# Kernel tuning notes

Measured on AMD Instinct MI355X. Metric: run time of the kernel, lower is better.

Reference implementation:

```python
import jax, jax.numpy as jnp
import numpy as np

# Dimensions
F = 512      # features = len(in_degrees)
D = 64
S, B, N = 1, 64, 256   # outer sample dim, hyper-batch, points per batch element
C = 128      # conditioner (phi) feature dim
P = F * F + F  # flat params per batch element: weight + bias


def _mask():
    # hidden-layer MADE degrees: arange(F) % max(1, D-1) + min(1, D-1)
    d = jnp.arange(F) % (D - 1) + 1
    # MaskedLinear hidden mask: out_degrees[:, None] >= in_degrees[None, :]
    # (the torch code reshapes the square [F,F] mask, which is an identity
    #  memory reshape, so element (i, j) = (d[i] >= d[j]))
    return (d[:, None] >= d[None, :]).astype(jnp.float32)


def setup_inputs() -> dict:
    key = jax.random.key(0)
    k1, k2, k3, k4 = jax.random.split(key, 4)
    return {
        "inputs": jax.random.normal(k1, (S, B, N, F), jnp.float32),
        "phi": jax.random.normal(k2, (S, B, C), jnp.float32),
        "Wc": jax.random.normal(k3, (P, C), jnp.float32) * 0.02,
        "bc": jax.random.normal(k4, (P,), jnp.float32) * 0.02,
    }


def reference(inputs, phi, Wc, bc):
    # Conditioner net: linear hypernetwork phi -> flat per-batch params.
    params = jnp.einsum('sbc,pc->sbp', phi, Wc) + bc          # [S,B,P]
    w = params[..., : F * F].reshape(S, B, F, F)               # [S,B,F_in,F_out]
    b = params[..., F * F : F * F + F]                         # [S,B,F]
    mw = w * _mask()                                           # masked per-batch weights

    # Residual block (no batch norm, dropout p=0): act -> masked linear (x2) -> residual
    t = jax.nn.relu(inputs)
    t = jnp.einsum('sbni,sbik->sbnk', t, mw) + b[:, :, None, :]
    t = jax.nn.relu(t)
    # Both MaskedLinear layers split the SAME conditioner output, so they share
    # (w, b); only the masks could differ, and with these degrees they coincide.
    t = jnp.einsum('sbni,sbik->sbnk', t, mw) + b[:, :, None, :]
    return inputs + t
```

## Files before the change

### kernel.cpp

```cpp
#include <hip/hip_runtime.h>
#include <hip/hip_bf16.h>

#define F_   512
#define FF_  (512 * 512)
#define C_   128

typedef __attribute__((ext_vector_type(4))) float f32x4;
typedef __attribute__((ext_vector_type(8))) short s16x8;
typedef __attribute__((ext_vector_type(4))) unsigned short u16x4;

__device__ __forceinline__ unsigned short f2bf(float f) {
    union { __hip_bfloat16 h; unsigned short u; } c;
    c.h = __float2bfloat16(f);
    return c.u;
}

__device__ __forceinline__ s16x8 pack8(f32x4 lo, f32x4 hi) {
    s16x8 r;
    r[0] = (short)f2bf(lo[0]); r[1] = (short)f2bf(lo[1]);
    r[2] = (short)f2bf(lo[2]); r[3] = (short)f2bf(lo[3]);
    r[4] = (short)f2bf(hi[0]); r[5] = (short)f2bf(hi[1]);
    r[6] = (short)f2bf(hi[2]); r[7] = (short)f2bf(hi[3]);
    return r;
}

#define GLDS16(gp, lp)                                                         \
    __builtin_amdgcn_global_load_lds(                                          \
        (const __attribute__((address_space(1))) void*)(gp),                   \
        (__attribute__((address_space(3))) void*)(lp), 16, 0, 0)

__global__ __launch_bounds__(256) void k0_prepack(
    const float* __restrict__ phi, unsigned short* __restrict__ phiP)
{
    const int t = threadIdx.x;
#pragma unroll
    for (int j = 0; j < 4; ++j) {
        int e = (j << 8) + t;
        int lane = e & 63, mk = e >> 6;
        int m = mk >> 2, kk = mk & 3;
        int brow = lane & 15, quad = lane >> 4;
        const float* p = phi + ((m << 4) + brow) * C_ + kk * 32 + (quad << 3);
        s16x8 v = pack8(*(const f32x4*)p, *(const f32x4*)(p + 4));
        *(s16x8*)&phiP[e << 3] = v;
    }
}

__global__ __launch_bounds__(256, 2) void k1_params(
    const unsigned short* __restrict__ phiP, const float* __restrict__ Wc,
    const float* __restrict__ bc, unsigned short* __restrict__ wT,
    float* __restrict__ biasWS, const float* __restrict__ phi)
{
    const int blk = blockIdx.x;
    const int tid = threadIdx.x;

    if (blk >= 512) {
        int g = ((blk - 512) << 8) + tid;
        int k = g >> 6, b = g & 63;
        const f32x4* w4 = (const f32x4*)(Wc + (size_t)(FF_ + k) * C_);
        const f32x4* p4 = (const f32x4*)(phi + b * C_);
        float acc = bc[FF_ + k];
#pragma unroll
        for (int c = 0; c < 32; ++c) {
            f32x4 a = w4[c], q = p4[c];
            acc += a[0]*q[0] + a[1]*q[1] + a[2]*q[2] + a[3]*q[3];
        }
        biasWS[(b << 9) + k] = acc;
        return;
    }

    __shared__ __align__(16) char stg[2][32768];
    __shared__ __align__(16) unsigned short trans[4][1280];
    __shared__ float bcs[64 * 9];

    const int lane = tid & 63, wave = tid >> 6, quad = lane >> 4;
    const int i0 = (blk >> 6) << 6;
    const int k0 = (blk & 63) << 3;

    {
        int il = tid >> 2, kp = (tid & 3) << 1;
        const float* s = bc + (size_t)(i0 + il) * F_ + k0 + kp;
        bcs[il * 9 + kp]     = s[0];
        bcs[il * 9 + kp + 1] = s[1];
    }

    s16x8 bfr[4];
#pragma unroll
    for (int kk = 0; kk < 4; ++kk)
        bfr[kk] = *(const s16x8*)&phiP[((((wave << 2) + kk) << 6) | lane) << 3];

    int dcell[4][4];
#pragma unroll
    for (int mt = 0; mt < 4; ++mt)
#pragma unroll
        for (int rr = 0; rr < 4; ++rr)
            dcell[mt][rr] = (i0 + mt * 16 + (quad << 2) + rr) % 63;
    int dmax[4];
#pragma unroll
    for (int mt = 0; mt < 4; ++mt) {
        int a = (i0 + mt * 16) % 63;
        dmax[mt] = (a + 15 >= 63) ? 62 : a + 15;
    }

    int irow[8], drow[8], swj[8];
#pragma unroll
    for (int j = 0; j < 8; ++j) {
        int rl = (wave << 4) + (j << 1) + (lane >> 5);
        irow[j] = i0 + rl;
        drow[j] = (i0 + rl) % 63;
        swj[j]  = ((lane & 31) << 4) ^ ((rl & 7) << 4);
    }
    const int idup = i0 + ((62 - (i0 % 63)) + 63) % 63;

    auto STAGE = [&](int t, int buf) {
        const int k = k0 + t, dk = (k0 + t) % 63;
#pragma unroll
        for (int j = 0; j < 8; ++j) {
            int isel = (drow[j] >= dk) ? irow[j] : idup;
            const char* src = (const char*)Wc
                            + ((size_t)(isel * F_ + k) << 9) + swj[j];
            GLDS16(src, stg[buf] + (((wave << 4) + (j << 1)) << 9));
        }
    };

    STAGE(0, 0);
    __syncthreads();

    const int swz = (lane & 7) << 4;

#pragma unroll
    for (int t = 0; t < 8; ++t) {
        if (t < 7) STAGE(t + 1, (t + 1) & 1);

        const int dk = (k0 + t) % 63;
        const char* sb = stg[t & 1];
        unsigned short* trw = trans[wave];

#pragma unroll
        for (int mt = 0; mt < 4; ++mt) {
            const int tpos = ((lane & 15) * 160
                           + ((mt * 32 + (quad << 3)) ^ swz)) >> 1;
            if (dmax[mt] >= dk) {
                f32x4 acc = (f32x4){0.f, 0.f, 0.f, 0.f};
                const char* rowb = sb + ((mt * 16 + (lane & 15)) << 9);
#pragma unroll
                for (int kk = 0; kk < 4; ++kk) {
                    int x = ((kk << 7) + (quad << 5)) ^ swz;
                    f32x4 lo = *(const f32x4*)(rowb + x);
                    f32x4 hi = *(const f32x4*)(rowb + (x ^ 16));
                    acc = __builtin_amdgcn_mfma_f32_16x16x32_bf16(
                        pack8(lo, hi), bfr[kk], acc, 0, 0, 0);
                }
                u16x4 v;
#pragma unroll
                for (int rr = 0; rr < 4; ++rr) {
                    float bv = bcs[(mt * 16 + (quad << 2) + rr) * 9 + t];
                    v[rr] = (dcell[mt][rr] >= dk)
                          ? f2bf(acc[rr] + bv) : (unsigned short)0;
                }
                *(u16x4*)&trw[tpos] = v;
            } else {
                *(u16x4*)&trw[tpos] = (u16x4){0, 0, 0, 0};
            }
        }

#pragma unroll
        for (int h = 0; h < 2; ++h) {
            int bl = (h << 3) + (lane >> 3), r = lane & 7;
            int rr2 = r ^ (bl & 7);
            s16x8 v = *(const s16x8*)&trw[bl * 80 + (rr2 << 3)];
            unsigned short* dst = wT
                + (((size_t)(((wave << 4) + bl) << 9) + k0 + t) << 9)
                + i0 + (r << 3);
            *(s16x8*)dst = v;
        }

        if (t < 7) {
            asm volatile("s_waitcnt vmcnt(2)" ::: "memory");
            __builtin_amdgcn_s_barrier();
        }
    }
}

#define SMEM_BOFF 66560
#define CHUNK_B   32768
#define SMEM_TOT  (66560 + 2 * 32768)

__global__ __launch_bounds__(512) void k2_apply(
    const float* __restrict__ X, const unsigned short* __restrict__ wT,
    const float* __restrict__ biasWS, float* __restrict__ out)
{
    extern __shared__ char smem[];
    unsigned short* A_lds = (unsigned short*)smem;

    const int blk = blockIdx.x;
    const int sw  = ((blk & 7) << 5) + (blk >> 3);
    const int b   = sw >> 2;
    const int n0  = (sw & 3) << 6;

    const int tid = threadIdx.x, lane = tid & 63, wave = tid >> 6;
    const int wn = wave >> 2, wk = wave & 3;

    const float* Xb = X + (((size_t)(b * 256 + n0)) << 9);
    float*       Ob = out + (((size_t)(b * 256 + n0)) << 9);
    const unsigned short* wTb = wT + ((size_t)b << 18);

    float biasr[8];
#pragma unroll
    for (int nt = 0; nt < 8; ++nt)
        biasr[nt] = biasWS[(b << 9) + (wk << 7) + (nt << 4) + (lane & 15)];

    {
        const f32x4* X4 = (const f32x4*)Xb;
#pragma unroll
        for (int j = 0; j < 16; ++j) {
            int f = (j << 9) + tid;
            int row = f >> 7, c4 = f & 127;
            f32x4 v = X4[f];
            u16x4 h;
#pragma unroll
            for (int e = 0; e < 4; ++e) h[e] = f2bf(fmaxf(v[e], 0.f));
            *(u16x4*)&A_lds[row * 520 + (c4 << 2)] = h;
        }
    }

    const int srcslot = ((lane & 3) ^ ((lane >> 3) & 3)) << 3;

    f32x4 acc[2][8];

    for (int phase = 0; phase < 2; ++phase) {
#pragma unroll
        for (int mt = 0; mt < 2; ++mt)
#pragma unroll
            for (int nt = 0; nt < 8; ++nt) acc[mt][nt] = (f32x4){0.f, 0.f, 0.f, 0.f};

#pragma unroll
        for (int g = 0; g < 4; ++g) {
            int krow = (wave << 6) + (g << 4) + (lane >> 2);
            const unsigned short* src = wTb + ((size_t)krow << 9) + srcslot;
            char* lp = smem + SMEM_BOFF + (((wave << 6) + (g << 4)) << 6);
            GLDS16(src, lp);
        }
        asm volatile("s_waitcnt vmcnt(0)" ::: "memory");
        __syncthreads();

        for (int c = 0; c < 16; ++c) {
            const int cur = c & 1;
            if (c < 15) {
                const int i0n = (c + 1) << 5;
#pragma unroll
                for (int g = 0; g < 4; ++g) {
                    int krow = (wave << 6) + (g << 4) + (lane >> 2);
                    const unsigned short* src = wTb + ((size_t)krow << 9) + i0n + srcslot;
                    char* lp = smem + SMEM_BOFF + (cur ^ 1) * CHUNK_B
                             + (((wave << 6) + (g << 4)) << 6);
                    GLDS16(src, lp);
                }
            }
            const int i0c = c << 5;
            s16x8 afr[2];
#pragma unroll
            for (int mt = 0; mt < 2; ++mt) {
                int n = (wn << 5) + (mt << 4) + (lane & 15);
                afr[mt] = *(const s16x8*)&A_lds[n * 520 + i0c + ((lane >> 4) << 3)];
            }
            const unsigned short* Bb =
                (const unsigned short*)(smem + SMEM_BOFF + cur * CHUNK_B);
#pragma unroll
            for (int nt = 0; nt < 8; ++nt) {
                int k = (wk << 7) + (nt << 4) + (lane & 15);
                int slot = (((lane >> 4) ^ ((k >> 1) & 3)) << 3);
                s16x8 bfr = *(const s16x8*)&Bb[(k << 5) + slot];
#pragma unroll
                for (int mt = 0; mt < 2; ++mt)
                    acc[mt][nt] = __builtin_amdgcn_mfma_f32_16x16x32_bf16(
                        afr[mt], bfr, acc[mt][nt], 0, 0, 0);
            }
            asm volatile("s_waitcnt vmcnt(0)" ::: "memory");
            __syncthreads();
        }

        if (phase == 0) {
#pragma unroll
            for (int mt = 0; mt < 2; ++mt)
#pragma unroll
                for (int nt = 0; nt < 8; ++nt) {
                    int k = (wk << 7) + (nt << 4) + (lane & 15);
#pragma unroll
                    for (int r = 0; r < 4; ++r) {
                        int n = (wn << 5) + (mt << 4) + ((lane >> 4) << 2) + r;
                        A_lds[n * 520 + k] =
                            f2bf(fmaxf(acc[mt][nt][r] + biasr[nt], 0.f));
                    }
                }
            __syncthreads();
        }
    }

#pragma unroll
    for (int mt = 0; mt < 2; ++mt)
#pragma unroll
        for (int nt = 0; nt < 8; ++nt) {
            int k = (wk << 7) + (nt << 4) + (lane & 15);
#pragma unroll
            for (int r = 0; r < 4; ++r) {
                int n = (wn << 5) + (mt << 4) + ((lane >> 4) << 2) + r;
                size_t off = ((size_t)n << 9) + k;
                Ob[off] = Xb[off] + acc[mt][nt][r] + biasr[nt];
            }
        }
}

extern "C" void kernel_launch(void* const* d_in, const int* in_sizes, int n_in,
                              void* d_out, int out_size, void* d_ws, size_t ws_size,
                              hipStream_t stream) {
    const float* inputs = (const float*)d_in[0];
    const float* phi    = (const float*)d_in[1];
    const float* Wc     = (const float*)d_in[2];
    const float* bc     = (const float*)d_in[3];
    float* out = (float*)d_out;

    unsigned short* wT = (unsigned short*)d_ws;
    float* biasWS = (float*)((char*)d_ws + (size_t)64 * 512 * 512 * 2);
    unsigned short* phiP =
        (unsigned short*)((char*)d_ws + (size_t)64 * 512 * 512 * 2 + 64 * 512 * 4);

    hipLaunchKernelGGL(k0_prepack, dim3(1), dim3(256), 0, stream, phi, phiP);

    hipLaunchKernelGGL(k1_params, dim3(640), dim3(256), 0, stream,
                       phiP, Wc, bc, wT, biasWS, phi);

    hipFuncSetAttribute((const void*)k2_apply,
                        hipFuncAttributeMaxDynamicSharedMemorySize, SMEM_TOT);
    hipLaunchKernelGGL(k2_apply, dim3(256), dim3(512), SMEM_TOT, stream,
                       inputs, wT, biasWS, out);
}
```

Before: 75.06 us.

## Pre-convert masked conditioner weights to swizzled bf16 layout before GEMM

```diff
diff --git a/kernel.cpp b/kernel.cpp
--- a/kernel.cpp
+++ b/kernel.cpp
@@ -45,42 +45,57 @@
     }
 }
 
-__global__ __launch_bounds__(256, 2) void k1_params(
-    const unsigned short* __restrict__ phiP, const float* __restrict__ Wc,
-    const float* __restrict__ bc, unsigned short* __restrict__ wT,
-    float* __restrict__ biasWS, const float* __restrict__ phi)
-{
-    const int blk = blockIdx.x;
-    const int tid = threadIdx.x;
-
-    if (blk >= 512) {
-        int g = ((blk - 512) << 8) + tid;
-        int k = g >> 6, b = g & 63;
-        const f32x4* w4 = (const f32x4*)(Wc + (size_t)(FF_ + k) * C_);
-        const f32x4* p4 = (const f32x4*)(phi + b * C_);
-        float acc = bc[FF_ + k];
-#pragma unroll
-        for (int c = 0; c < 32; ++c) {
-            f32x4 a = w4[c], q = p4[c];
-            acc += a[0]*q[0] + a[1]*q[1] + a[2]*q[2] + a[3]*q[3];
-        }
-        biasWS[(b << 9) + k] = acc;
-        return;
-    }
-
-    __shared__ __align__(16) char stg[2][32768];
+__global__ __launch_bounds__(256) void kT(
+    const float* __restrict__ Wc, unsigned short* __restrict__ Wc2)
+{
+    size_t gid = ((size_t)blockIdx.x << 8) + threadIdx.x;
+    int p = (int)(gid >> 4), u = (int)(gid & 15);
+    int i = p >> 9, k = p & 511;
+    s16x8 v;
+    if ((i % 63) >= (k % 63)) {
+        const float* src = Wc + ((size_t)p << 7) + (u << 3);
+        v = pack8(*(const f32x4*)src, *(const f32x4*)(src + 4));
+    } else {
+        v = (s16x8){0, 0, 0, 0, 0, 0, 0, 0};
+    }
+    int up = u ^ (i & 7);
+    *(s16x8*)&Wc2[(((size_t)((k << 9) | i)) << 7) + (up << 3)] = v;
+}
+
+__global__ __launch_bounds__(256) void k1c_bias(
+    const float* __restrict__ phi, const float* __restrict__ Wc,
+    const float* __restrict__ bc, float* __restrict__ biasWS)
+{
+    int g = (blockIdx.x << 8) + threadIdx.x;
+    int k = g >> 6, b = g & 63;
+    const f32x4* w4 = (const f32x4*)(Wc + (size_t)(FF_ + k) * C_);
+    const f32x4* p4 = (const f32x4*)(phi + b * C_);
+    float acc = bc[FF_ + k];
+#pragma unroll
+    for (int c = 0; c < 32; ++c) {
+        f32x4 a = w4[c], q = p4[c];
+        acc += a[0]*q[0] + a[1]*q[1] + a[2]*q[2] + a[3]*q[3];
+    }
+    biasWS[(b << 9) + k] = acc;
+}
+
+__global__ __launch_bounds__(256, 3) void k1b_gemm(
+    const unsigned short* __restrict__ phiP,
+    const unsigned short* __restrict__ Wc2,
+    const float* __restrict__ bc, unsigned short* __restrict__ wT)
+{
+    __shared__ __align__(16) char stg[2][16384];
     __shared__ __align__(16) unsigned short trans[4][1280];
-    __shared__ float bcs[64 * 9];
-
-    const int lane = tid & 63, wave = tid >> 6, quad = lane >> 4;
-    const int i0 = (blk >> 6) << 6;
-    const int k0 = (blk & 63) << 3;
+    __shared__ float bcs[64 * 5];
+
+    const int tid = threadIdx.x, lane = tid & 63, wave = tid >> 6;
+    const int quad = lane >> 4;
+    const int i0 = (blockIdx.x >> 7) << 6;
+    const int k0 = (blockIdx.x & 127) << 2;
 
     {
-        int il = tid >> 2, kp = (tid & 3) << 1;
-        const float* s = bc + (size_t)(i0 + il) * F_ + k0 + kp;
-        bcs[il * 9 + kp]     = s[0];
-        bcs[il * 9 + kp + 1] = s[1];
+        int il = tid >> 2, kp = tid & 3;
+        bcs[il * 5 + kp] = bc[(size_t)(i0 + il) * F_ + k0 + kp];
     }
 
     s16x8 bfr[4];
@@ -101,35 +116,27 @@
         dmax[mt] = (a + 15 >= 63) ? 62 : a + 15;
     }
 
-    int irow[8], drow[8], swj[8];
-#pragma unroll
-    for (int j = 0; j < 8; ++j) {
-        int rl = (wave << 4) + (j << 1) + (lane >> 5);
-        irow[j] = i0 + rl;
-        drow[j] = (i0 + rl) % 63;
-        swj[j]  = ((lane & 31) << 4) ^ ((rl & 7) << 4);
-    }
-    const int idup = i0 + ((62 - (i0 % 63)) + 63) % 63;
-
     auto STAGE = [&](int t, int buf) {
-        const int k = k0 + t, dk = (k0 + t) % 63;
-#pragma unroll
-        for (int j = 0; j < 8; ++j) {
-            int isel = (drow[j] >= dk) ? irow[j] : idup;
-            const char* src = (const char*)Wc
-                            + ((size_t)(isel * F_ + k) << 9) + swj[j];
-            GLDS16(src, stg[buf] + (((wave << 4) + (j << 1)) << 9));
+        const int k = k0 + t;
+#pragma unroll
+        for (int j = 0; j < 4; ++j) {
+            const int r0 = (wave << 4) + (j << 2);
+            const char* src = (const char*)Wc2
+                            + (((size_t)((k << 9) + i0 + r0)) << 8)
+                            + (lane << 4);
+            GLDS16(src, stg[buf] + (r0 << 8));
         }
     };
 
     STAGE(0, 0);
+    asm volatile("s_waitcnt vmcnt(0)" ::: "memory");
     __syncthreads();
 
-    const int swz = (lane & 7) << 4;
-
-#pragma unroll
-    for (int t = 0; t < 8; ++t) {
-        if (t < 7) STAGE(t + 1, (t + 1) & 1);
+    const int swz = lane & 7;
+
+#pragma unroll
+    for (int t = 0; t < 4; ++t) {
+        if (t < 3) STAGE(t + 1, (t + 1) & 1);
 
         const int dk = (k0 + t) % 63;
         const char* sb = stg[t & 1];
@@ -138,22 +145,22 @@
 #pragma unroll
         for (int mt = 0; mt < 4; ++mt) {
             const int tpos = ((lane & 15) * 160
-                           + ((mt * 32 + (quad << 3)) ^ swz)) >> 1;
+                           + ((mt * 32 + (quad << 3)) ^ ((lane & 7) << 4))) >> 1;
             if (dmax[mt] >= dk) {
                 f32x4 acc = (f32x4){0.f, 0.f, 0.f, 0.f};
-                const char* rowb = sb + ((mt * 16 + (lane & 15)) << 9);
+                const int row = mt * 16 + (lane & 15);
+                const char* rowb = sb + (row << 8);
 #pragma unroll
                 for (int kk = 0; kk < 4; ++kk) {
-                    int x = ((kk << 7) + (quad << 5)) ^ swz;
-                    f32x4 lo = *(const f32x4*)(rowb + x);
-                    f32x4 hi = *(const f32x4*)(rowb + (x ^ 16));
+                    int u = ((kk << 2) + quad) ^ swz;
+                    s16x8 afr = *(const s16x8*)(rowb + (u << 4));
                     acc = __builtin_amdgcn_mfma_f32_16x16x32_bf16(
-                        pack8(lo, hi), bfr[kk], acc, 0, 0, 0);
+                        afr, bfr[kk], acc, 0, 0, 0);
                 }
                 u16x4 v;
 #pragma unroll
                 for (int rr = 0; rr < 4; ++rr) {
-                    float bv = bcs[(mt * 16 + (quad << 2) + rr) * 9 + t];
+                    float bv = bcs[(mt * 16 + (quad << 2) + rr) * 5 + t];
                     v[rr] = (dcell[mt][rr] >= dk)
                           ? f2bf(acc[rr] + bv) : (unsigned short)0;
                 }
@@ -169,12 +176,12 @@
             int rr2 = r ^ (bl & 7);
             s16x8 v = *(const s16x8*)&trw[bl * 80 + (rr2 << 3)];
             unsigned short* dst = wT
-                + (((size_t)(((wave << 4) + bl) << 9) + k0 + t) << 9)
+                + (((size_t)((((wave << 4) + bl) << 9) + k0 + t)) << 9)
                 + i0 + (r << 3);
             *(s16x8*)dst = v;
         }
 
-        if (t < 7) {
+        if (t < 3) {
             asm volatile("s_waitcnt vmcnt(2)" ::: "memory");
             __builtin_amdgcn_s_barrier();
         }
@@ -323,11 +330,15 @@
     float* biasWS = (float*)((char*)d_ws + (size_t)64 * 512 * 512 * 2);
     unsigned short* phiP =
         (unsigned short*)((char*)d_ws + (size_t)64 * 512 * 512 * 2 + 64 * 512 * 4);
+    unsigned short* Wc2 =
+        (unsigned short*)((char*)d_ws + ((size_t)64 << 20));
 
     hipLaunchKernelGGL(k0_prepack, dim3(1), dim3(256), 0, stream, phi, phiP);
-
-    hipLaunchKernelGGL(k1_params, dim3(640), dim3(256), 0, stream,
-                       phiP, Wc, bc, wT, biasWS, phi);
+    hipLaunchKernelGGL(kT, dim3(16384), dim3(256), 0, stream, Wc, Wc2);
+    hipLaunchKernelGGL(k1c_bias, dim3(128), dim3(256), 0, stream,
+                       phi, Wc, bc, biasWS);
+    hipLaunchKernelGGL(k1b_gemm, dim3(1024), dim3(256), 0, stream,
+                       phiP, Wc2, bc, wT);
 
     hipFuncSetAttribute((const void*)k2_apply,
                         hipFuncAttributeMaxDynamicSharedMemorySize, SMEM_TOT);
```

Measured after the change: 95.53 us. 1.27x slower.
